# Kernel optimization log

Measured on AMD Instinct MI355X. Metric: run time of the kernel, lower is better.

## Reference

```python
import jax, jax.numpy as jnp
import numpy as np

D, H, S, L = 256, 512, 32, 2  # latent_dim, hidden_dim, stochastic_dim, n_layers
B, T = 256, 256


def setup_inputs() -> dict:
    key = jax.random.key(0)
    ks = jax.random.split(key, 20)

    def w(k, shape, fan_in):
        return jax.random.uniform(k, shape, jnp.float32, -1.0, 1.0) / np.sqrt(fan_in)

    inp = {
        "latent": jax.random.normal(ks[0], (B, T, D), jnp.float32),
        "hidden": jnp.zeros((L, B, H), jnp.float32),
        "eps": jax.random.normal(ks[1], (B, T, S), jnp.float32),
        # GRU layer 0: input = D + S
        "wih0": w(ks[2], (3 * H, D + S), H), "whh0": w(ks[3], (3 * H, H), H),
        "bih0": w(ks[4], (3 * H,), H), "bhh0": w(ks[5], (3 * H,), H),
        # GRU layer 1: input = H
        "wih1": w(ks[6], (3 * H, H), H), "whh1": w(ks[7], (3 * H, H), H),
        "bih1": w(ks[8], (3 * H,), H), "bhh1": w(ks[9], (3 * H,), H),
        # posterior MLP: (H + D) -> H -> 2S
        "wpost1": w(ks[10], (H, H + D), H + D), "bpost1": w(ks[11], (H,), H + D),
        "wpost2": w(ks[12], (2 * S, H), H), "bpost2": w(ks[13], (2 * S,), H),
        # prior MLP: H -> H -> 2S
        "wprior1": w(ks[14], (H, H), H), "bprior1": w(ks[15], (H,), H),
        "wprior2": w(ks[16], (2 * S, H), H), "bprior2": w(ks[17], (2 * S,), H),
    }
    return inp


def _gru_cell(x, h, wih, whh, bih, bhh):
    gi = x @ wih.T + bih   # [B, 3H]
    gh = h @ whh.T + bhh   # [B, 3H]
    ir, iz, inn = jnp.split(gi, 3, axis=-1)
    hr, hz, hn = jnp.split(gh, 3, axis=-1)
    r = jax.nn.sigmoid(ir + hr)
    z = jax.nn.sigmoid(iz + hz)
    n = jnp.tanh(inn + r * hn)
    return (1.0 - z) * n + z * h


def reference(latent, hidden, eps,
              wih0, whh0, bih0, bhh0, wih1, whh1, bih1, bhh1,
              wpost1, bpost1, wpost2, bpost2, wprior1, bprior1, wprior2, bprior2):
    # scan over time; carry = hidden [L, B, H]
    def step(h, xs):
        x_t, e_t = xs  # [B,D], [B,S]
        post_in = jnp.concatenate([h[-1], x_t], axis=-1)           # [B, H+D]
        pp = jax.nn.relu(post_in @ wpost1.T + bpost1) @ wpost2.T + bpost2
        pm, plv = jnp.split(pp, 2, axis=-1)                        # [B,S] each
        stoch = pm + e_t * jnp.exp(0.5 * plv)                      # reparam sample
        rnn_in = jnp.concatenate([x_t, stoch], axis=-1)            # [B, D+S]
        h0 = _gru_cell(rnn_in, h[0], wih0, whh0, bih0, bhh0)
        h1 = _gru_cell(h0, h[1], wih1, whh1, bih1, bhh1)
        h_new = jnp.stack([h0, h1], axis=0)                        # [L,B,H]
        pr = jax.nn.relu(h1 @ wprior1.T + bprior1) @ wprior2.T + bprior2
        prm, prlv = jnp.split(pr, 2, axis=-1)
        return h_new, (stoch, prm, prlv, pm, plv)

    xs = (jnp.swapaxes(latent, 0, 1), jnp.swapaxes(eps, 0, 1))     # [T,B,*]
    h_final, outs = jax.lax.scan(step, hidden, xs)
    stoch, prm, prlv, pm, plv = (jnp.swapaxes(o, 0, 1) for o in outs)  # [B,T,*]
    return stoch, prm, prlv, pm, plv, h_final
```

## Files before the change

kernel.cpp:

```cpp
#include <hip/hip_runtime.h>
#include <math.h>

#define TID ((int)threadIdx.x)

namespace {

constexpr int Bn = 256, Tn = 256, Dn = 256, Hn = 512, Sn = 32;
constexpr int NOS = 32;
constexpr int JH  = 16;
constexpr int BC  = 32;
constexpr int BTS = Bn * Tn * Sn;
constexpr int OFF_ST   = 0;
constexpr int OFF_PRM  = BTS;
constexpr int OFF_PRLV = 2 * BTS;
constexpr int OFF_PM   = 3 * BTS;
constexpr int OFF_PLV  = 4 * BTS;
constexpr int OFF_HF   = 5 * BTS;
constexpr int BARS_PER_TEAM = 1056;

struct P {
  const float *latent, *hidden, *eps;
  const float *wih0, *whh0, *bih0, *bhh0;
  const float *wih1, *whh1, *bih1, *bhh1;
  const float *wpost1, *bpost1, *wpost2, *bpost2;
  const float *wprior1, *bprior1, *wprior2, *bprior2;
  float *out;
  float *h0, *h1, *ph, *qh, *st;
  unsigned *bars;
};

__device__ __forceinline__ void team_bar(unsigned* slot) {
  __syncthreads();
  if (TID == 0) {
    __threadfence();
    __hip_atomic_fetch_add(slot, 1u, __ATOMIC_RELEASE, __HIP_MEMORY_SCOPE_AGENT);
    while (__hip_atomic_load(slot, __ATOMIC_ACQUIRE, __HIP_MEMORY_SCOPE_AGENT) < 32u) {
      __builtin_amdgcn_s_sleep(1);
    }
  }
  __syncthreads();
}

template<int SHIFT>
__device__ __forceinline__ void stageW48(float (*wT)[52], const float* __restrict__ W,
                                         int K, int k0, int os) {
  constexpr int KQ = 1 << SHIFT;
  const int nf4 = 48 * KQ;
  for (int v = TID; v < nf4; v += 512) {
    const int row = v >> SHIFT;
    const int kq  = v & (KQ - 1);
    const int g = row >> 4, j = row & 15;
    const float4 w = *(const float4*)(W + (size_t)(g * Hn + os * JH + j) * K + k0 + (kq << 2));
    const int kk = kq << 2;
    wT[kk + 0][row] = w.x; wT[kk + 1][row] = w.y;
    wT[kk + 2][row] = w.z; wT[kk + 3][row] = w.w;
  }
}

__device__ __forceinline__ void stageW16(float (*wT)[52], int co, const float* __restrict__ W,
                                         int K, int wrow0, int k0) {
  for (int v = TID; v < 256; v += 512) {
    const int j = v >> 4;
    const int kq = v & 15;
    const float4 w = *(const float4*)(W + (size_t)(wrow0 + j) * K + k0 + (kq << 2));
    const int kk = kq << 2;
    wT[kk + 0][co + j] = w.x; wT[kk + 1][co + j] = w.y;
    wT[kk + 2][co + j] = w.z; wT[kk + 3][co + j] = w.w;
  }
}

template<int SHIFT>
__device__ __forceinline__ void stageX(float (*xc)[68], const float* __restrict__ src,
                                       int rstride, int k0, int bg) {
  constexpr int KQ = 1 << SHIFT;
  const int nf4 = 32 * KQ;
  for (int v = TID; v < nf4; v += 512) {
    const int row = v >> SHIFT;
    const int kq = v & (KQ - 1);
    const float4 x = *(const float4*)(src + (size_t)(bg * BC + row) * rstride + k0 + (kq << 2));
    *(float4*)&xc[row][kq << 2] = x;
  }
}

__device__ __forceinline__ void ghAccum(float* acc, const float (*wT)[52], const float (*xc)[68],
                                        int v, int ka, int kb) {
  const int rp = v >> 3, jp = v & 7;
  const int r0 = rp * 2, c0 = jp * 2;
  #pragma unroll 4
  for (int kk = ka; kk < kb; kk += 2) {
    const float2 xa = *(const float2*)&xc[r0][kk];
    const float2 xb = *(const float2*)&xc[r0 + 1][kk];
    #pragma unroll
    for (int g = 0; g < 3; g++) {
      const float2 w0 = *(const float2*)&wT[kk][g * 16 + c0];
      const float2 w1 = *(const float2*)&wT[kk + 1][g * 16 + c0];
      acc[g * 4 + 0] += xa.x * w0.x + xa.y * w1.x;
      acc[g * 4 + 1] += xa.x * w0.y + xa.y * w1.y;
      acc[g * 4 + 2] += xb.x * w0.x + xb.y * w1.x;
      acc[g * 4 + 3] += xb.x * w0.y + xb.y * w1.y;
    }
  }
}

__device__ __forceinline__ void qAccum(float* acc, const float (*wT)[52], int co,
                                       const float (*xc)[68], int v, int ka, int kb) {
  const int rp = v >> 3, jp = v & 7;
  const int r0 = rp * 2, c0 = jp * 2;
  #pragma unroll 4
  for (int kk = ka; kk < kb; kk += 2) {
    const float2 xa = *(const float2*)&xc[r0][kk];
    const float2 xb = *(const float2*)&xc[r0 + 1][kk];
    const float2 w0 = *(const float2*)&wT[kk][co + c0];
    const float2 w1 = *(const float2*)&wT[kk + 1][co + c0];
    acc[0] += xa.x * w0.x + xa.y * w1.x;
    acc[1] += xa.x * w0.y + xa.y * w1.y;
    acc[2] += xb.x * w0.x + xb.y * w1.x;
    acc[3] += xb.x * w0.y + xb.y * w1.y;
  }
}

__device__ __forceinline__ float dotChunk(const float* __restrict__ x, const float* __restrict__ w,
                                          int k0, int n) {
  float d = 0.f;
  #pragma unroll 4
  for (int k = k0; k < k0 + n; k += 4) {
    const float4 a = *(const float4*)(x + k);
    const float4 b = *(const float4*)(w + k);
    d += a.x * b.x + a.y * b.y + a.z * b.z + a.w * b.w;
  }
  return d;
}

__global__ __launch_bounds__(512, 1) void rssm_kernel(P p) {
  __shared__ float wT0[64][52];
  __shared__ float wT1[64][52];
  __shared__ float xcA[32][68];
  __shared__ float xcB[32][68];
  __shared__ float ghA[32][48];
  __shared__ float ghB[32][48];
  __shared__ float part[4][32][48];
  __shared__ float ppq[2][2][32];
  __shared__ float prq[2][2][32];
  __shared__ float ppv[32][2];

  const int bg = blockIdx.x & 7;
  const int os = blockIdx.x >> 3;
  unsigned* bars = p.bars + bg * BARS_PER_TEAM;
  int bar_i = 0;

  const int wv = TID >> 6;
  const int v  = TID & 127;
  const int wp = TID >> 7;

  {
    const int r = TID >> 4, j = TID & 15;
    const int b = bg * BC + r; const int col = os * JH + j;
    p.h0[b * Hn + col] = p.hidden[b * Hn + col];
    p.h1[b * Hn + col] = p.hidden[Bn * Hn + b * Hn + col];
  }
  team_bar(&bars[bar_i++]);

  auto phaseE = [&](int tnext) {
    float acc[4] = {0.f, 0.f, 0.f, 0.f};
    const bool do_ph = (tnext < Tn);
    const int nch = do_ph ? 12 : 8;
    for (int c = 0; c < nch; c++) {
      const int k0 = c << 6;
      if (c < 8) {
        stageW16(wT0, 0, p.wprior1, Hn, os * JH, k0);
        stageX<4>(xcA, p.h1, Hn, k0, bg);
      } else {
        stageX<4>(xcA, p.latent + (size_t)tnext * Dn, Tn * Dn, k0 - Hn, bg);
      }
      if (do_ph) stageW16(wT0, 16, p.wpost1, Hn + Dn, os * JH, k0);
      __syncthreads();
      if (wp < 2) { if (c < 8) qAccum(acc, wT0, 0, xcA, v, wp * 32, wp * 32 + 32); }
      else if (do_ph) qAccum(acc, wT0, 16, xcA, v, (wp - 2) * 32, (wp - 2) * 32 + 32);
      __syncthreads();
    }
    float* pE = &part[0][0][0];
    {
      const int rp = v >> 3, jp = v & 7;
      pE[(wp * 32 + rp * 2    ) * 16 + jp * 2    ] = acc[0];
      pE[(wp * 32 + rp * 2    ) * 16 + jp * 2 + 1] = acc[1];
      pE[(wp * 32 + rp * 2 + 1) * 16 + jp * 2    ] = acc[2];
      pE[(wp * 32 + rp * 2 + 1) * 16 + jp * 2 + 1] = acc[3];
    }
    __syncthreads();
    {
      const int r = TID >> 4, j = TID & 15;
      const int b = bg * BC + r; const int col = os * JH + j;
      const float qv = pE[r * 16 + j] + pE[(32 + r) * 16 + j] + p.bprior1[col];
      p.qh[b * Hn + col] = fmaxf(qv, 0.f);
      if (do_ph) {
        const float pv = pE[(64 + r) * 16 + j] + pE[(96 + r) * 16 + j] + p.bpost1[col];
        p.ph[b * Hn + col] = fmaxf(pv, 0.f);
      }
    }
    __syncthreads();
  };

  auto phaseB = [&](int t) {
    float acc[12] = {0,0,0,0,0,0,0,0,0,0,0,0};
    float dacc = 0.f;
    const int ll = TID & 127;
    const int r_ = ll & 31, cc_ = (ll >> 5) & 1, ks_ = ll >> 6;
    for (int c = 0; c < 8; c++) {
      const int k0 = c << 6;
      stageW48<4>(wT0, p.whh0, Hn, k0, os);
      stageW48<4>(wT1, p.whh1, Hn, k0, os);
      stageX<4>(xcA, p.h0, Hn, k0, bg);
      stageX<4>(xcB, p.h1, Hn, k0, bg);
      __syncthreads();
      if (wv < 2)      ghAccum(acc, wT0, xcA, v, 0, 64);
      else if (wv < 4) ghAccum(acc, wT1, xcB, v, 0, 64);
      else if (wv < 6)
        dacc += dotChunk(p.ph + (size_t)(bg * BC + r_) * Hn,
                         p.wpost2 + (size_t)(os + 32 * cc_) * Hn, ks_ * 256 + c * 32, 32);
      else if (t >= 1)
        dacc += dotChunk(p.qh + (size_t)(bg * BC + r_) * Hn,
                         p.wprior2 + (size_t)(os + 32 * cc_) * Hn, ks_ * 256 + c * 32, 32);
      __syncthreads();
    }
    if (wv < 4) {
      const int rp = v >> 3, jp = v & 7;
      float (*gh)[48] = (wv < 2) ? ghA : ghB;
      const float* bias = (wv < 2) ? p.bhh0 : p.bhh1;
      #pragma unroll
      for (int g = 0; g < 3; g++) {
        const int col = os * JH + jp * 2;
        gh[rp * 2    ][g * 16 + jp * 2    ] = acc[g * 4 + 0] + bias[g * Hn + col];
        gh[rp * 2    ][g * 16 + jp * 2 + 1] = acc[g * 4 + 1] + bias[g * Hn + col + 1];
        gh[rp * 2 + 1][g * 16 + jp * 2    ] = acc[g * 4 + 2] + bias[g * Hn + col];
        gh[rp * 2 + 1][g * 16 + jp * 2 + 1] = acc[g * 4 + 3] + bias[g * Hn + col + 1];
      }
    } else if (wv < 6) {
      ppq[cc_][ks_][r_] = dacc;
    } else if (t >= 1) {
      prq[cc_][ks_][r_] = dacc;
    }
    __syncthreads();
    if (TID < 64) {
      const int r = TID & 31, cc = TID >> 5;
      ppv[r][cc] = ppq[cc][0][r] + ppq[cc][1][r] + p.bpost2[os + 32 * cc];
    } else if (TID < 128 && t >= 1) {
      const int u = TID - 64; const int r = u & 31, cc = u >> 5;
      const float val = prq[cc][0][r] + prq[cc][1][r] + p.bprior2[os + 32 * cc];
      p.out[(cc ? OFF_PRLV : OFF_PRM) + (size_t)(bg * BC + r) * (Tn * Sn) + (t - 1) * Sn + os] = val;
    }
    __syncthreads();
    if (TID < 32) {
      const int r = TID; const int b = bg * BC + r;
      const float pm = ppv[r][0], plv = ppv[r][1];
      const float e = p.eps[(size_t)b * (Tn * Sn) + t * Sn + os];
      const float sv = pm + e * expf(0.5f * plv);
      p.st[b * Sn + os] = sv;
      p.out[OFF_ST  + (size_t)b * (Tn * Sn) + t * Sn + os] = sv;
      p.out[OFF_PM  + (size_t)b * (Tn * Sn) + t * Sn + os] = pm;
      p.out[OFF_PLV + (size_t)b * (Tn * Sn) + t * Sn + os] = plv;
    }
    __syncthreads();
  };

  auto phaseGRU = [&](const float* W, const float* bih, float (*ghL)[48], float* hbuf,
                      bool layer0, int t) {
    float acc[12] = {0,0,0,0,0,0,0,0,0,0,0,0};
    const int nch = layer0 ? 5 : 8;
    for (int c = 0; c < nch; c++) {
      const int k0 = c << 6;
      int klen;
      if (layer0) {
        if (c < 4) { stageW48<4>(wT0, W, Dn + Sn, k0, os);
                     stageX<4>(xcA, p.latent + (size_t)t * Dn, Tn * Dn, k0, bg); klen = 64; }
        else       { stageW48<3>(wT0, W, Dn + Sn, k0, os);
                     stageX<3>(xcA, p.st, Sn, 0, bg); klen = 32; }
      } else {
        stageW48<4>(wT0, W, Hn, k0, os);
        stageX<4>(xcA, p.h0, Hn, k0, bg); klen = 64;
      }
      __syncthreads();
      const int q = klen >> 2;
      ghAccum(acc, wT0, xcA, v, wp * q, wp * q + q);
      __syncthreads();
    }
    {
      const int rp = v >> 3, jp = v & 7;
      #pragma unroll
      for (int g = 0; g < 3; g++) {
        part[wp][rp * 2    ][g * 16 + jp * 2    ] = acc[g * 4 + 0];
        part[wp][rp * 2    ][g * 16 + jp * 2 + 1] = acc[g * 4 + 1];
        part[wp][rp * 2 + 1][g * 16 + jp * 2    ] = acc[g * 4 + 2];
        part[wp][rp * 2 + 1][g * 16 + jp * 2 + 1] = acc[g * 4 + 3];
      }
    }
    __syncthreads();
    {
      const int r = TID >> 4, j = TID & 15;
      const int b = bg * BC + r; const int col = os * JH + j;
      const float ig0 = part[0][r][j] + part[1][r][j] + part[2][r][j] + part[3][r][j] + bih[col];
      const float ig1 = part[0][r][16 + j] + part[1][r][16 + j] + part[2][r][16 + j] + part[3][r][16 + j] + bih[Hn + col];
      const float ig2 = part[0][r][32 + j] + part[1][r][32 + j] + part[2][r][32 + j] + part[3][r][32 + j] + bih[2 * Hn + col];
      const float hr = ghL[r][j], hz = ghL[r][16 + j], hn = ghL[r][32 + j];
      const float rg = 1.f / (1.f + expf(-(ig0 + hr)));
      const float zg = 1.f / (1.f + expf(-(ig1 + hz)));
      const float ng = tanhf(ig2 + rg * hn);
      const float hold = hbuf[b * Hn + col];
      hbuf[b * Hn + col] = (1.f - zg) * ng + zg * hold;
    }
    __syncthreads();
  };

  phaseE(0);
  team_bar(&bars[bar_i++]);

  for (int t = 0; t < Tn; t++) {
    phaseB(t);
    team_bar(&bars[bar_i++]);
    phaseGRU(p.wih0, p.bih0, ghA, p.h0, true, t);
    team_bar(&bars[bar_i++]);
    phaseGRU(p.wih1, p.bih1, ghB, p.h1, false, t);
    team_bar(&bars[bar_i++]);
    phaseE(t + 1);
    team_bar(&bars[bar_i++]);
  }

  {
    const int ll = TID & 127;
    const int r_ = ll & 31, cc_ = (ll >> 5) & 1, ks_ = ll >> 6;
    if (wv >= 6) {
      const float d = dotChunk(p.qh + (size_t)(bg * BC + r_) * Hn,
                               p.wprior2 + (size_t)(os + 32 * cc_) * Hn, ks_ * 256, 256);
      prq[cc_][ks_][r_] = d;
    }
    __syncthreads();
    if (TID >= 64 && TID < 128) {
      const int u = TID - 64; const int r = u & 31, cc = u >> 5;
      const float val = prq[cc][0][r] + prq[cc][1][r] + p.bprior2[os + 32 * cc];
      p.out[(cc ? OFF_PRLV : OFF_PRM) + (size_t)(bg * BC + r) * (Tn * Sn) + 255 * Sn + os] = val;
    }
    const int r = TID >> 4, j = TID & 15;
    const int b = bg * BC + r; const int col = os * JH + j;
    p.out[OFF_HF + b * Hn + col] = p.h0[b * Hn + col];
    p.out[OFF_HF + Bn * Hn + b * Hn + col] = p.h1[b * Hn + col];
  }
}

}

extern "C" void kernel_launch(void* const* d_in, const int* in_sizes, int n_in,
                              void* d_out, int out_size, void* d_ws, size_t ws_size,
                              hipStream_t stream) {
  (void)in_sizes; (void)n_in; (void)out_size; (void)ws_size;
  float* ws = (float*)d_ws;
  P p;
  p.latent  = (const float*)d_in[0];
  p.hidden  = (const float*)d_in[1];
  p.eps     = (const float*)d_in[2];
  p.wih0    = (const float*)d_in[3];
  p.whh0    = (const float*)d_in[4];
  p.bih0    = (const float*)d_in[5];
  p.bhh0    = (const float*)d_in[6];
  p.wih1    = (const float*)d_in[7];
  p.whh1    = (const float*)d_in[8];
  p.bih1    = (const float*)d_in[9];
  p.bhh1    = (const float*)d_in[10];
  p.wpost1  = (const float*)d_in[11];
  p.bpost1  = (const float*)d_in[12];
  p.wpost2  = (const float*)d_in[13];
  p.bpost2  = (const float*)d_in[14];
  p.wprior1 = (const float*)d_in[15];
  p.bprior1 = (const float*)d_in[16];
  p.wprior2 = (const float*)d_in[17];
  p.bprior2 = (const float*)d_in[18];
  p.out = (float*)d_out;
  p.h0 = ws;
  p.h1 = ws + 131072;
  p.ph = ws + 262144;
  p.qh = ws + 393216;
  p.st = ws + 524288;
  p.bars = (unsigned*)(ws + 532480);

  hipMemsetAsync(p.bars, 0, 8 * BARS_PER_TEAM * sizeof(unsigned), stream);

  void* args[] = { &p };
  hipLaunchCooperativeKernel((void*)rssm_kernel, dim3(256), dim3(512), args, 0, stream);
}
```

Baseline: 33.18 ms.

## Keep per-block weight slices resident in LDS and restructure team partitioning

Repartitions the work so each of 256 blocks owns 4 hidden columns for one of 2 batch halves of 128 rows. All of that block's weight slices (GRU input and hidden weights, post/prior first layers, one head row) are preloaded into dynamic LDS once, instead of being restaged from global memory every chunk of every timestep. Activations are streamed in 32-wide chunks that are double-buffered through registers, and the K split is reduced with a shuffle butterfly. The per-step flat atomic barrier with a fresh slot each time is replaced by a two-level tree barrier that counts epochs. The trade-off is a large LDS footprint and a 128-block team spin barrier, which may cost more synchronisation latency.

```diff
diff --git a/kernel.cpp b/kernel.cpp
--- a/kernel.cpp
+++ b/kernel.cpp
@@ -6,17 +6,25 @@
 namespace {
 
 constexpr int Bn = 256, Tn = 256, Dn = 256, Hn = 512, Sn = 32;
-constexpr int NOS = 32;
-constexpr int JH  = 16;
-constexpr int BC  = 32;
+constexpr int BC = 128;
+constexpr int XP = 268;
+constexpr int CHF = 16 * XP;
 constexpr int BTS = Bn * Tn * Sn;
-constexpr int OFF_ST   = 0;
-constexpr int OFF_PRM  = BTS;
-constexpr int OFF_PRLV = 2 * BTS;
-constexpr int OFF_PM   = 3 * BTS;
-constexpr int OFF_PLV  = 4 * BTS;
-constexpr int OFF_HF   = 5 * BTS;
-constexpr int BARS_PER_TEAM = 1056;
+constexpr int OFF_ST = 0, OFF_PRM = BTS, OFF_PRLV = 2 * BTS, OFF_PM = 3 * BTS,
+              OFF_PLV = 4 * BTS, OFF_HF = 5 * BTS;
+
+constexpr int oWH0 = 0;
+constexpr int oWH1 = oWH0 + 512 * 12;
+constexpr int oWI1 = oWH1 + 512 * 12;
+constexpr int oWI0 = oWI1 + 512 * 12;
+constexpr int oWP1 = oWI0 + 288 * 12;
+constexpr int oWQ1 = oWP1 + 768 * 4;
+constexpr int oWHD = oWQ1 + 512 * 4;
+constexpr int oGA  = oWHD + 512;
+constexpr int oGB  = oGA + 128 * 12;
+constexpr int oXT  = oGB + 128 * 12;
+constexpr int LDS_FLOATS = oXT + 2 * CHF;
+constexpr int LDS_BYTES  = LDS_FLOATS * 4;
 
 struct P {
   const float *latent, *hidden, *eps;
@@ -25,323 +33,395 @@
   const float *wpost1, *bpost1, *wpost2, *bpost2;
   const float *wprior1, *bprior1, *wprior2, *bprior2;
   float *out;
-  float *h0, *h1, *ph, *qh, *st;
+  float *h0, *h1, *ph, *qh, *ppv;
   unsigned *bars;
 };
 
-__device__ __forceinline__ void team_bar(unsigned* slot) {
+struct F4x2 { float4 a, b; };
+struct SR { float4 pm0, pm1, lv0, lv1, e0, e1; };
+
+__device__ __forceinline__ void team_bar(const P& p, int bg, int grp, int e) {
   __syncthreads();
   if (TID == 0) {
-    __threadfence();
-    __hip_atomic_fetch_add(slot, 1u, __ATOMIC_RELEASE, __HIP_MEMORY_SCOPE_AGENT);
-    while (__hip_atomic_load(slot, __ATOMIC_ACQUIRE, __HIP_MEMORY_SCOPE_AGENT) < 32u) {
-      __builtin_amdgcn_s_sleep(1);
-    }
+    unsigned* leaf = p.bars + bg * 8 + grp;
+    unsigned* root = p.bars + 16 + bg;
+    unsigned* rel  = p.bars + 18 + bg;
+    unsigned old = __hip_atomic_fetch_add(leaf, 1u, __ATOMIC_RELEASE, __HIP_MEMORY_SCOPE_AGENT);
+    if ((old & 15u) == 15u) {
+      unsigned r = __hip_atomic_fetch_add(root, 1u, __ATOMIC_ACQ_REL, __HIP_MEMORY_SCOPE_AGENT);
+      if ((r & 7u) == 7u)
+        __hip_atomic_store(rel, (unsigned)e, __ATOMIC_RELEASE, __HIP_MEMORY_SCOPE_AGENT);
+    }
+    while (__hip_atomic_load(rel, __ATOMIC_RELAXED, __HIP_MEMORY_SCOPE_AGENT) < (unsigned)e)
+      __builtin_amdgcn_s_sleep(2);
+    (void)__hip_atomic_load(rel, __ATOMIC_ACQUIRE, __HIP_MEMORY_SCOPE_AGENT);
   }
   __syncthreads();
 }
 
-template<int SHIFT>
-__device__ __forceinline__ void stageW48(float (*wT)[52], const float* __restrict__ W,
-                                         int K, int k0, int os) {
-  constexpr int KQ = 1 << SHIFT;
-  const int nf4 = 48 * KQ;
-  for (int v = TID; v < nf4; v += 512) {
-    const int row = v >> SHIFT;
-    const int kq  = v & (KQ - 1);
-    const int g = row >> 4, j = row & 15;
-    const float4 w = *(const float4*)(W + (size_t)(g * Hn + os * JH + j) * K + k0 + (kq << 2));
-    const int kk = kq << 2;
-    wT[kk + 0][row] = w.x; wT[kk + 1][row] = w.y;
-    wT[kk + 2][row] = w.z; wT[kk + 3][row] = w.w;
-  }
-}
-
-__device__ __forceinline__ void stageW16(float (*wT)[52], int co, const float* __restrict__ W,
-                                         int K, int wrow0, int k0) {
-  for (int v = TID; v < 256; v += 512) {
-    const int j = v >> 4;
-    const int kq = v & 15;
-    const float4 w = *(const float4*)(W + (size_t)(wrow0 + j) * K + k0 + (kq << 2));
-    const int kk = kq << 2;
-    wT[kk + 0][co + j] = w.x; wT[kk + 1][co + j] = w.y;
-    wT[kk + 2][co + j] = w.z; wT[kk + 3][co + j] = w.w;
-  }
-}
-
-template<int SHIFT>
-__device__ __forceinline__ void stageX(float (*xc)[68], const float* __restrict__ src,
-                                       int rstride, int k0, int bg) {
-  constexpr int KQ = 1 << SHIFT;
-  const int nf4 = 32 * KQ;
-  for (int v = TID; v < nf4; v += 512) {
-    const int row = v >> SHIFT;
-    const int kq = v & (KQ - 1);
-    const float4 x = *(const float4*)(src + (size_t)(bg * BC + row) * rstride + k0 + (kq << 2));
-    *(float4*)&xc[row][kq << 2] = x;
-  }
-}
-
-__device__ __forceinline__ void ghAccum(float* acc, const float (*wT)[52], const float (*xc)[68],
-                                        int v, int ka, int kb) {
-  const int rp = v >> 3, jp = v & 7;
-  const int r0 = rp * 2, c0 = jp * 2;
-  #pragma unroll 4
-  for (int kk = ka; kk < kb; kk += 2) {
-    const float2 xa = *(const float2*)&xc[r0][kk];
-    const float2 xb = *(const float2*)&xc[r0 + 1][kk];
-    #pragma unroll
-    for (int g = 0; g < 3; g++) {
-      const float2 w0 = *(const float2*)&wT[kk][g * 16 + c0];
-      const float2 w1 = *(const float2*)&wT[kk + 1][g * 16 + c0];
-      acc[g * 4 + 0] += xa.x * w0.x + xa.y * w1.x;
-      acc[g * 4 + 1] += xa.x * w0.y + xa.y * w1.y;
-      acc[g * 4 + 2] += xb.x * w0.x + xb.y * w1.x;
-      acc[g * 4 + 3] += xb.x * w0.y + xb.y * w1.y;
-    }
-  }
-}
-
-__device__ __forceinline__ void qAccum(float* acc, const float (*wT)[52], int co,
-                                       const float (*xc)[68], int v, int ka, int kb) {
-  const int rp = v >> 3, jp = v & 7;
-  const int r0 = rp * 2, c0 = jp * 2;
-  #pragma unroll 4
-  for (int kk = ka; kk < kb; kk += 2) {
-    const float2 xa = *(const float2*)&xc[r0][kk];
-    const float2 xb = *(const float2*)&xc[r0 + 1][kk];
-    const float2 w0 = *(const float2*)&wT[kk][co + c0];
-    const float2 w1 = *(const float2*)&wT[kk + 1][co + c0];
-    acc[0] += xa.x * w0.x + xa.y * w1.x;
-    acc[1] += xa.x * w0.y + xa.y * w1.y;
-    acc[2] += xb.x * w0.x + xb.y * w1.x;
-    acc[3] += xb.x * w0.y + xb.y * w1.y;
-  }
-}
-
-__device__ __forceinline__ float dotChunk(const float* __restrict__ x, const float* __restrict__ w,
-                                          int k0, int n) {
-  float d = 0.f;
-  #pragma unroll 4
-  for (int k = k0; k < k0 + n; k += 4) {
-    const float4 a = *(const float4*)(x + k);
-    const float4 b = *(const float4*)(w + k);
-    d += a.x * b.x + a.y * b.y + a.z * b.z + a.w * b.w;
-  }
-  return d;
-}
-
-__global__ __launch_bounds__(512, 1) void rssm_kernel(P p) {
-  __shared__ float wT0[64][52];
-  __shared__ float wT1[64][52];
-  __shared__ float xcA[32][68];
-  __shared__ float xcB[32][68];
-  __shared__ float ghA[32][48];
-  __shared__ float ghB[32][48];
-  __shared__ float part[4][32][48];
-  __shared__ float ppq[2][2][32];
-  __shared__ float prq[2][2][32];
-  __shared__ float ppv[32][2];
-
-  const int bg = blockIdx.x & 7;
-  const int os = blockIdx.x >> 3;
-  unsigned* bars = p.bars + bg * BARS_PER_TEAM;
-  int bar_i = 0;
-
-  const int wv = TID >> 6;
-  const int v  = TID & 127;
-  const int wp = TID >> 7;
-
+template<int K>
+__device__ void preload12(float* wt, const float* __restrict__ W, int os) {
+  constexpr int KQ = K / 4;
+  for (int u = TID; u < 12 * KQ; u += 512) {
+    int c = u / KQ, kq = u - c * KQ;
+    int row = (c >> 2) * Hn + os * 4 + (c & 3);
+    float4 w = *(const float4*)(W + (size_t)row * K + kq * 4);
+    int k = kq * 4;
+    wt[(k + 0) * 12 + c] = w.x; wt[(k + 1) * 12 + c] = w.y;
+    wt[(k + 2) * 12 + c] = w.z; wt[(k + 3) * 12 + c] = w.w;
+  }
+}
+template<int K>
+__device__ void preload4(float* wt, const float* __restrict__ W, int os) {
+  constexpr int KQ = K / 4;
+  for (int u = TID; u < 4 * KQ; u += 512) {
+    int c = u / KQ, kq = u - c * KQ;
+    int row = os * 4 + c;
+    float4 w = *(const float4*)(W + (size_t)row * K + kq * 4);
+    int k = kq * 4;
+    wt[(k + 0) * 4 + c] = w.x; wt[(k + 1) * 4 + c] = w.y;
+    wt[(k + 2) * 4 + c] = w.z; wt[(k + 3) * 4 + c] = w.w;
+  }
+}
+
+__device__ __forceinline__ F4x2 stLoad(const float* __restrict__ src, size_t ld, int k0) {
+  F4x2 v;
+  const int r0 = TID >> 3, kq = TID & 7;
+  v.a = *(const float4*)(src + (size_t)r0 * ld + k0 + kq * 4);
+  v.b = *(const float4*)(src + (size_t)(r0 + 64) * ld + k0 + kq * 4);
+  return v;
+}
+__device__ __forceinline__ void stWrite(float* __restrict__ xb, const F4x2& v) {
+  const int r0 = TID >> 3, kq = TID & 7;
+  *(float2*)&xb[(2 * kq) * XP + 2 * r0]       = make_float2(v.a.x, v.a.y);
+  *(float2*)&xb[(2 * kq + 1) * XP + 2 * r0]   = make_float2(v.a.z, v.a.w);
+  *(float2*)&xb[(2 * kq) * XP + 2 * (r0 + 64)]     = make_float2(v.b.x, v.b.y);
+  *(float2*)&xb[(2 * kq + 1) * XP + 2 * (r0 + 64)] = make_float2(v.b.z, v.b.w);
+}
+
+__device__ __forceinline__ void mm12(float* __restrict__ acc, const float* __restrict__ xb,
+                                     const float* __restrict__ wt, int rp, int ks) {
+  const float4 xa = *(const float4*)&xb[ks * XP + rp * 8];
+  const float4 xc = *(const float4*)&xb[ks * XP + rp * 8 + 4];
+  const float* w = wt + ks * 24;
+  float wA[12], wB[12];
+  #pragma unroll
+  for (int c = 0; c < 12; c += 4) {
+    *(float4*)&wA[c] = *(const float4*)&w[c];
+    *(float4*)&wB[c] = *(const float4*)&w[12 + c];
+  }
+  const float x0[4] = {xa.x, xa.z, xc.x, xc.z};
+  const float x1[4] = {xa.y, xa.w, xc.y, xc.w};
+  #pragma unroll
+  for (int ri = 0; ri < 4; ri++)
+    #pragma unroll
+    for (int c = 0; c < 12; c++)
+      acc[ri * 12 + c] += x0[ri] * wA[c] + x1[ri] * wB[c];
+}
+
+template<bool DP>
+__device__ __forceinline__ void mmE(float* __restrict__ acc, const float* __restrict__ xb,
+                                    const float* __restrict__ wq, const float* __restrict__ wp,
+                                    int rp, int ks) {
+  const float4 xa = *(const float4*)&xb[ks * XP + rp * 8];
+  const float4 xc = *(const float4*)&xb[ks * XP + rp * 8 + 4];
+  const float x0[4] = {xa.x, xa.z, xc.x, xc.z};
+  const float x1[4] = {xa.y, xa.w, xc.y, xc.w};
+  const float4 q0 = *(const float4*)&wq[ks * 8];
+  const float4 q1 = *(const float4*)&wq[ks * 8 + 4];
+  const float qA[4] = {q0.x, q0.y, q0.z, q0.w};
+  const float qB[4] = {q1.x, q1.y, q1.z, q1.w};
+  float pA[4] = {0, 0, 0, 0}, pB[4] = {0, 0, 0, 0};
+  if (DP) {
+    const float4 p0 = *(const float4*)&wp[ks * 8];
+    const float4 p1 = *(const float4*)&wp[ks * 8 + 4];
+    pA[0] = p0.x; pA[1] = p0.y; pA[2] = p0.z; pA[3] = p0.w;
+    pB[0] = p1.x; pB[1] = p1.y; pB[2] = p1.z; pB[3] = p1.w;
+  }
+  #pragma unroll
+  for (int ri = 0; ri < 4; ri++)
+    #pragma unroll
+    for (int c = 0; c < 4; c++) {
+      acc[ri * 8 + c] += x0[ri] * qA[c] + x1[ri] * qB[c];
+      if (DP) acc[ri * 8 + 4 + c] += x0[ri] * pA[c] + x1[ri] * pB[c];
+    }
+}
+
+__device__ __forceinline__ void mmEpost(float* __restrict__ acc, const float* __restrict__ xb,
+                                        const float* __restrict__ wp, int rp, int ks) {
+  const float4 xa = *(const float4*)&xb[ks * XP + rp * 8];
+  const float4 xc = *(const float4*)&xb[ks * XP + rp * 8 + 4];
+  const float x0[4] = {xa.x, xa.z, xc.x, xc.z};
+  const float x1[4] = {xa.y, xa.w, xc.y, xc.w};
+  const float4 p0 = *(const float4*)&wp[ks * 8];
+  const float4 p1 = *(const float4*)&wp[ks * 8 + 4];
+  const float pA[4] = {p0.x, p0.y, p0.z, p0.w};
+  const float pB[4] = {p1.x, p1.y, p1.z, p1.w};
+  #pragma unroll
+  for (int ri = 0; ri < 4; ri++)
+    #pragma unroll
+    for (int c = 0; c < 4; c++)
+      acc[ri * 8 + 4 + c] += x0[ri] * pA[c] + x1[ri] * pB[c];
+}
+
+template<int N>
+__device__ __forceinline__ void bfly(float* acc) {
+  #pragma unroll
+  for (int m = 1; m <= 8; m <<= 1)
+    #pragma unroll
+    for (int i = 0; i < N; i++)
+      acc[i] += __shfl_xor(acc[i], m, 64);
+}
+
+__global__ __launch_bounds__(512, 2) void rssm_kernel(P p) {
+  extern __shared__ float sm[];
+  const int bg = blockIdx.x & 1;
+  const int os = blockIdx.x >> 1;
+  const int grp = os & 7;
+  const int rp = TID >> 4, ks = TID & 15;
+  int ep = 0;
+
+  float* WH0 = sm + oWH0; float* WH1 = sm + oWH1; float* WI1 = sm + oWI1;
+  float* WI0 = sm + oWI0; float* WP1 = sm + oWP1; float* WQ1 = sm + oWQ1;
+  float* WHD = sm + oWHD; float* GA = sm + oGA;  float* GB = sm + oGB;
+  auto XT = [&](int i) { return sm + oXT + i * CHF; };
+
+  preload12<512>(WH0, p.whh0, os);
+  preload12<512>(WH1, p.whh1, os);
+  preload12<512>(WI1, p.wih1, os);
+  preload12<288>(WI0, p.wih0, os);
+  preload4<768>(WP1, p.wpost1, os);
+  preload4<512>(WQ1, p.wprior1, os);
   {
-    const int r = TID >> 4, j = TID & 15;
-    const int b = bg * BC + r; const int col = os * JH + j;
-    p.h0[b * Hn + col] = p.hidden[b * Hn + col];
-    p.h1[b * Hn + col] = p.hidden[Bn * Hn + b * Hn + col];
-  }
-  team_bar(&bars[bar_i++]);
-
-  auto phaseE = [&](int tnext) {
-    float acc[4] = {0.f, 0.f, 0.f, 0.f};
-    const bool do_ph = (tnext < Tn);
-    const int nch = do_ph ? 12 : 8;
+    const float* hw = (os < 64) ? (p.wpost2 + (size_t)os * Hn)
+                                : (p.wprior2 + (size_t)(os - 64) * Hn);
+    for (int u = TID; u < 128; u += 512)
+      *(float4*)&WHD[u * 4] = *(const float4*)(hw + u * 4);
+  }
+  {
+    const int r = TID >> 2, j = TID & 3;
+    const int b = bg * BC + r, col = os * 4 + j;
+    p.h0[(size_t)b * Hn + col] = p.hidden[(size_t)b * Hn + col];
+    p.h1[(size_t)b * Hn + col] = p.hidden[(size_t)Bn * Hn + b * Hn + col];
+  }
+  team_bar(p, bg, grp, ++ep);
+
+  auto runMM12 = [&](float* acc, const float* src, size_t ld, const float* wt, int nch) {
+    F4x2 nxt;
+    { F4x2 cur = stLoad(src, ld, 0);
+      if (nch > 1) nxt = stLoad(src, ld, 32);
+      stWrite(XT(0), cur); }
+    __syncthreads();
     for (int c = 0; c < nch; c++) {
-      const int k0 = c << 6;
-      if (c < 8) {
-        stageW16(wT0, 0, p.wprior1, Hn, os * JH, k0);
-        stageX<4>(xcA, p.h1, Hn, k0, bg);
+      F4x2 fut;
+      if (c + 2 < nch) fut = stLoad(src, ld, (c + 2) * 32);
+      mm12(acc, XT(c & 1), wt + c * 32 * 12, rp, ks);
+      if (c + 1 < nch) stWrite(XT((c + 1) & 1), nxt);
+      __syncthreads();
+      nxt = fut;
+    }
+  };
+
+  auto writeG = [&](float* G, const float* acc, const float* bhh) {
+    if (ks < 12) {
+      const int c = ks, g = c >> 2, j = c & 3;
+      const float bb = bhh[g * Hn + os * 4 + j];
+      #pragma unroll
+      for (int i = 0; i < 4; i++) G[(rp * 4 + i) * 12 + c] = acc[i * 12 + c] + bb;
+    }
+  };
+
+  auto combine = [&](const float* acc, const float* G, float* hbuf, const float* bih) {
+    if (ks < 4) {
+      const int j = ks, col = os * 4 + j;
+      const float b0 = bih[col], b1 = bih[Hn + col], b2 = bih[2 * Hn + col];
+      #pragma unroll
+      for (int i = 0; i < 4; i++) {
+        const int r = rp * 4 + i, b = bg * BC + r;
+        const float gr = acc[i * 12 + j] + b0 + G[r * 12 + j];
+        const float gz = acc[i * 12 + 4 + j] + b1 + G[r * 12 + 4 + j];
+        const float gn = acc[i * 12 + 8 + j] + b2;
+        const float hnv = G[r * 12 + 8 + j];
+        const float rg = 1.f / (1.f + expf(-gr));
+        const float zg = 1.f / (1.f + expf(-gz));
+        const float ng = tanhf(gn + rg * hnv);
+        const size_t idx = (size_t)b * Hn + col;
+        hbuf[idx] = (1.f - zg) * ng + zg * hbuf[idx];
+      }
+    }
+  };
+
+  auto headPhase = [&](int t, bool post) {
+    const int r = TID >> 2, kq = TID & 3;
+    const int b = bg * BC + r;
+    const float* xs = (post ? p.ph : p.qh) + (size_t)b * Hn;
+    float d = 0.f;
+    #pragma unroll
+    for (int q = 0; q < 32; q++) {
+      const int k = kq * 128 + q * 4;
+      const float4 xv = *(const float4*)(xs + k);
+      const float4 wv = *(const float4*)&WHD[k];
+      d += xv.x * wv.x + xv.y * wv.y + xv.z * wv.z + xv.w * wv.w;
+    }
+    d += __shfl_xor(d, 1, 64);
+    d += __shfl_xor(d, 2, 64);
+    if (kq == 0) {
+      if (post) {
+        const float val = d + p.bpost2[os];
+        p.ppv[(size_t)b * 64 + os] = val;
+        const size_t o = ((size_t)b * Tn + t) * Sn + (os & 31);
+        p.out[(os < 32 ? OFF_PM : OFF_PLV) + o] = val;
       } else {
-        stageX<4>(xcA, p.latent + (size_t)tnext * Dn, Tn * Dn, k0 - Hn, bg);
+        const int cc = os - 64;
+        const float val = d + p.bprior2[cc];
+        const size_t o = ((size_t)b * Tn + (t - 1)) * Sn + (cc & 31);
+        p.out[(cc < 32 ? OFF_PRM : OFF_PRLV) + o] = val;
       }
-      if (do_ph) stageW16(wT0, 16, p.wpost1, Hn + Dn, os * JH, k0);
+    }
+  };
+
+  auto stochLoad = [&](SR& s, int t) {
+    const int r = TID >> 2, sq = TID & 3;
+    const int b = bg * BC + r;
+    const float* pv = p.ppv + (size_t)b * 64;
+    s.pm0 = *(const float4*)(pv + sq * 8);
+    s.pm1 = *(const float4*)(pv + sq * 8 + 4);
+    s.lv0 = *(const float4*)(pv + 32 + sq * 8);
+    s.lv1 = *(const float4*)(pv + 32 + sq * 8 + 4);
+    const float* epp = p.eps + ((size_t)b * Tn + t) * Sn + sq * 8;
+    s.e0 = *(const float4*)epp;
+    s.e1 = *(const float4*)(epp + 4);
+  };
+  auto stochWrite = [&](float* xb, const SR& s, int t) {
+    const int r = TID >> 2, sq = TID & 3;
+    const int b = bg * BC + r;
+    const float pm[8] = {s.pm0.x, s.pm0.y, s.pm0.z, s.pm0.w, s.pm1.x, s.pm1.y, s.pm1.z, s.pm1.w};
+    const float lv[8] = {s.lv0.x, s.lv0.y, s.lv0.z, s.lv0.w, s.lv1.x, s.lv1.y, s.lv1.z, s.lv1.w};
+    const float ev[8] = {s.e0.x, s.e0.y, s.e0.z, s.e0.w, s.e1.x, s.e1.y, s.e1.z, s.e1.w};
+    float sv[8];
+    #pragma unroll
+    for (int u = 0; u < 8; u++) sv[u] = pm[u] + ev[u] * expf(0.5f * lv[u]);
+    #pragma unroll
+    for (int up = 0; up < 4; up++) {
+      const int s2 = sq * 4 + up;
+      *(float2*)&xb[s2 * XP + 2 * r] = make_float2(sv[up * 2], sv[up * 2 + 1]);
+    }
+    if (os == 0) {
+      #pragma unroll
+      for (int u = 0; u < 8; u++)
+        p.out[OFF_ST + ((size_t)b * Tn + t) * Sn + sq * 8 + u] = sv[u];
+    }
+  };
+
+  auto phaseE = [&](int tn) {
+    const bool dp = (tn < Tn);
+    const int nch = dp ? 24 : 16;
+    const float* s1 = p.h1 + (size_t)bg * BC * Hn;
+    const float* slat = p.latent + (size_t)bg * BC * (size_t)(Tn * Dn) + (size_t)(dp ? tn : 0) * Dn;
+    auto eload = [&](int c) -> F4x2 {
+      return (c < 16) ? stLoad(s1, Hn, c * 32)
+                      : stLoad(slat, (size_t)Tn * Dn, (c - 16) * 32);
+    };
+    float acc[32] = {};
+    F4x2 nxt;
+    { F4x2 cur = eload(0); nxt = eload(1); stWrite(XT(0), cur); }
+    __syncthreads();
+    for (int c = 0; c < nch; c++) {
+      F4x2 fut;
+      if (c + 2 < nch) fut = eload(c + 2);
+      const float* xb = XT(c & 1);
+      if (c < 16) {
+        if (dp) mmE<true>(acc, xb, WQ1 + c * 32 * 4, WP1 + c * 32 * 4, rp, ks);
+        else    mmE<false>(acc, xb, WQ1 + c * 32 * 4, nullptr, rp, ks);
+      } else {
+        mmEpost(acc, xb, WP1 + c * 32 * 4, rp, ks);
+      }
+      if (c + 1 < nch) stWrite(XT((c + 1) & 1), nxt);
       __syncthreads();
-      if (wp < 2) { if (c < 8) qAccum(acc, wT0, 0, xcA, v, wp * 32, wp * 32 + 32); }
-      else if (do_ph) qAccum(acc, wT0, 16, xcA, v, (wp - 2) * 32, (wp - 2) * 32 + 32);
+      nxt = fut;
+    }
+    bfly<32>(acc);
+    if (ks < 4) {
+      const int col = os * 4 + ks;
+      const float bq = p.bprior1[col];
+      #pragma unroll
+      for (int i = 0; i < 4; i++)
+        p.qh[(size_t)(bg * BC + rp * 4 + i) * Hn + col] = fmaxf(acc[i * 8 + ks] + bq, 0.f);
+    } else if (ks < 8 && dp) {
+      const int j = ks - 4, col = os * 4 + j;
+      const float bp = p.bpost1[col];
+      #pragma unroll
+      for (int i = 0; i < 4; i++)
+        p.ph[(size_t)(bg * BC + rp * 4 + i) * Hn + col] = fmaxf(acc[i * 8 + 4 + j] + bp, 0.f);
+    }
+  };
+
+  auto phaseB = [&](int t) {
+    {
+      float acc[48] = {};
+      runMM12(acc, p.h0 + (size_t)bg * BC * Hn, Hn, WH0, 16);
+      bfly<48>(acc);
+      writeG(GA, acc, p.bhh0);
+    }
+    {
+      float acc[48] = {};
+      runMM12(acc, p.h1 + (size_t)bg * BC * Hn, Hn, WH1, 16);
+      bfly<48>(acc);
+      writeG(GB, acc, p.bhh1);
+    }
+    if (os < 64) headPhase(t, true);
+    else if (t >= 1) headPhase(t, false);
+  };
+
+  auto phaseC = [&](int t) {
+    const float* slat = p.latent + (size_t)bg * BC * (size_t)(Tn * Dn) + (size_t)t * Dn;
+    const size_t ldl = (size_t)Tn * Dn;
+    float acc[48] = {};
+    SR sreg;
+    F4x2 nxt;
+    { F4x2 cur = stLoad(slat, ldl, 0); nxt = stLoad(slat, ldl, 32); stWrite(XT(0), cur); }
+    __syncthreads();
+    for (int c = 0; c <= 8; c++) {
+      F4x2 fut;
+      if (c + 2 < 8) fut = stLoad(slat, ldl, (c + 2) * 32);
+      else if (c + 2 == 8) stochLoad(sreg, t);
+      mm12(acc, XT(c & 1), WI0 + c * 32 * 12, rp, ks);
+      if (c + 1 < 8) stWrite(XT((c + 1) & 1), nxt);
+      else if (c + 1 == 8) stochWrite(XT(0), sreg, t);
       __syncthreads();
-    }
-    float* pE = &part[0][0][0];
-    {
-      const int rp = v >> 3, jp = v & 7;
-      pE[(wp * 32 + rp * 2    ) * 16 + jp * 2    ] = acc[0];
-      pE[(wp * 32 + rp * 2    ) * 16 + jp * 2 + 1] = acc[1];
-      pE[(wp * 32 + rp * 2 + 1) * 16 + jp * 2    ] = acc[2];
-      pE[(wp * 32 + rp * 2 + 1) * 16 + jp * 2 + 1] = acc[3];
-    }
-    __syncthreads();
-    {
-      const int r = TID >> 4, j = TID & 15;
-      const int b = bg * BC + r; const int col = os * JH + j;
-      const float qv = pE[r * 16 + j] + pE[(32 + r) * 16 + j] + p.bprior1[col];
-      p.qh[b * Hn + col] = fmaxf(qv, 0.f);
-      if (do_ph) {
-        const float pv = pE[(64 + r) * 16 + j] + pE[(96 + r) * 16 + j] + p.bpost1[col];
-        p.ph[b * Hn + col] = fmaxf(pv, 0.f);
-      }
-    }
-    __syncthreads();
-  };
-
-  auto phaseB = [&](int t) {
-    float acc[12] = {0,0,0,0,0,0,0,0,0,0,0,0};
-    float dacc = 0.f;
-    const int ll = TID & 127;
-    const int r_ = ll & 31, cc_ = (ll >> 5) & 1, ks_ = ll >> 6;
-    for (int c = 0; c < 8; c++) {
-      const int k0 = c << 6;
-      stageW48<4>(wT0, p.whh0, Hn, k0, os);
-      stageW48<4>(wT1, p.whh1, Hn, k0, os);
-      stageX<4>(xcA, p.h0, Hn, k0, bg);
-      stageX<4>(xcB, p.h1, Hn, k0, bg);
-      __syncthreads();
-      if (wv < 2)      ghAccum(acc, wT0, xcA, v, 0, 64);
-      else if (wv < 4) ghAccum(acc, wT1, xcB, v, 0, 64);
-      else if (wv < 6)
-        dacc += dotChunk(p.ph + (size_t)(bg * BC + r_) * Hn,
-                         p.wpost2 + (size_t)(os + 32 * cc_) * Hn, ks_ * 256 + c * 32, 32);
-      else if (t >= 1)
-        dacc += dotChunk(p.qh + (size_t)(bg * BC + r_) * Hn,
-                         p.wprior2 + (size_t)(os + 32 * cc_) * Hn, ks_ * 256 + c * 32, 32);
-      __syncthreads();
-    }
-    if (wv < 4) {
-      const int rp = v >> 3, jp = v & 7;
-      float (*gh)[48] = (wv < 2) ? ghA : ghB;
-      const float* bias = (wv < 2) ? p.bhh0 : p.bhh1;
-      #pragma unroll
-      for (int g = 0; g < 3; g++) {
-        const int col = os * JH + jp * 2;
-        gh[rp * 2    ][g * 16 + jp * 2    ] = acc[g * 4 + 0] + bias[g * Hn + col];
-        gh[rp * 2    ][g * 16 + jp * 2 + 1] = acc[g * 4 + 1] + bias[g * Hn + col + 1];
-        gh[rp * 2 + 1][g * 16 + jp * 2    ] = acc[g * 4 + 2] + bias[g * Hn + col];
-        gh[rp * 2 + 1][g * 16 + jp * 2 + 1] = acc[g * 4 + 3] + bias[g * Hn + col + 1];
-      }
-    } else if (wv < 6) {
-      ppq[cc_][ks_][r_] = dacc;
-    } else if (t >= 1) {
-      prq[cc_][ks_][r_] = dacc;
-    }
-    __syncthreads();
-    if (TID < 64) {
-      const int r = TID & 31, cc = TID >> 5;
-      ppv[r][cc] = ppq[cc][0][r] + ppq[cc][1][r] + p.bpost2[os + 32 * cc];
-    } else if (TID < 128 && t >= 1) {
-      const int u = TID - 64; const int r = u & 31, cc = u >> 5;
-      const float val = prq[cc][0][r] + prq[cc][1][r] + p.bprior2[os + 32 * cc];
-      p.out[(cc ? OFF_PRLV : OFF_PRM) + (size_t)(bg * BC + r) * (Tn * Sn) + (t - 1) * Sn + os] = val;
-    }
-    __syncthreads();
-    if (TID < 32) {
-      const int r = TID; const int b = bg * BC + r;
-      const float pm = ppv[r][0], plv = ppv[r][1];
-      const float e = p.eps[(size_t)b * (Tn * Sn) + t * Sn + os];
-      const float sv = pm + e * expf(0.5f * plv);
-      p.st[b * Sn + os] = sv;
-      p.out[OFF_ST  + (size_t)b * (Tn * Sn) + t * Sn + os] = sv;
-      p.out[OFF_PM  + (size_t)b * (Tn * Sn) + t * Sn + os] = pm;
-      p.out[OFF_PLV + (size_t)b * (Tn * Sn) + t * Sn + os] = plv;
-    }
-    __syncthreads();
-  };
-
-  auto phaseGRU = [&](const float* W, const float* bih, float (*ghL)[48], float* hbuf,
-                      bool layer0, int t) {
-    float acc[12] = {0,0,0,0,0,0,0,0,0,0,0,0};
-    const int nch = layer0 ? 5 : 8;
-    for (int c = 0; c < nch; c++) {
-      const int k0 = c << 6;
-      int klen;
-      if (layer0) {
-        if (c < 4) { stageW48<4>(wT0, W, Dn + Sn, k0, os);
-                     stageX<4>(xcA, p.latent + (size_t)t * Dn, Tn * Dn, k0, bg); klen = 64; }
-        else       { stageW48<3>(wT0, W, Dn + Sn, k0, os);
-                     stageX<3>(xcA, p.st, Sn, 0, bg); klen = 32; }
-      } else {
-        stageW48<4>(wT0, W, Hn, k0, os);
-        stageX<4>(xcA, p.h0, Hn, k0, bg); klen = 64;
-      }
-      __syncthreads();
-      const int q = klen >> 2;
-      ghAccum(acc, wT0, xcA, v, wp * q, wp * q + q);
-      __syncthreads();
-    }
-    {
-      const int rp = v >> 3, jp = v & 7;
-      #pragma unroll
-      for (int g = 0; g < 3; g++) {
-        part[wp][rp * 2    ][g * 16 + jp * 2    ] = acc[g * 4 + 0];
-        part[wp][rp * 2    ][g * 16 + jp * 2 + 1] = acc[g * 4 + 1];
-        part[wp][rp * 2 + 1][g * 16 + jp * 2    ] = acc[g * 4 + 2];
-        part[wp][rp * 2 + 1][g * 16 + jp * 2 + 1] = acc[g * 4 + 3];
-      }
-    }
-    __syncthreads();
-    {
-      const int r = TID >> 4, j = TID & 15;
-      const int b = bg * BC + r; const int col = os * JH + j;
-      const float ig0 = part[0][r][j] + part[1][r][j] + part[2][r][j] + part[3][r][j] + bih[col];
-      const float ig1 = part[0][r][16 + j] + part[1][r][16 + j] + part[2][r][16 + j] + part[3][r][16 + j] + bih[Hn + col];
-      const float ig2 = part[0][r][32 + j] + part[1][r][32 + j] + part[2][r][32 + j] + part[3][r][32 + j] + bih[2 * Hn + col];
-      const float hr = ghL[r][j], hz = ghL[r][16 + j], hn = ghL[r][32 + j];
-      const float rg = 1.f / (1.f + expf(-(ig0 + hr)));
-      const float zg = 1.f / (1.f + expf(-(ig1 + hz)));
-      const float ng = tanhf(ig2 + rg * hn);
-      const float hold = hbuf[b * Hn + col];
-      hbuf[b * Hn + col] = (1.f - zg) * ng + zg * hold;
-    }
-    __syncthreads();
+      nxt = fut;
+    }
+    bfly<48>(acc);
+    combine(acc, GA, p.h0, p.bih0);
+  };
+
+  auto phaseD = [&]() {
+    float acc[48] = {};
+    runMM12(acc, p.h0 + (size_t)bg * BC * Hn, Hn, WI1, 16);
+    bfly<48>(acc);
+    combine(acc, GB, p.h1, p.bih1);
   };
 
   phaseE(0);
-  team_bar(&bars[bar_i++]);
+  team_bar(p, bg, grp, ++ep);
 
   for (int t = 0; t < Tn; t++) {
     phaseB(t);
-    team_bar(&bars[bar_i++]);
-    phaseGRU(p.wih0, p.bih0, ghA, p.h0, true, t);
-    team_bar(&bars[bar_i++]);
-    phaseGRU(p.wih1, p.bih1, ghB, p.h1, false, t);
-    team_bar(&bars[bar_i++]);
+    team_bar(p, bg, grp, ++ep);
+    phaseC(t);
+    team_bar(p, bg, grp, ++ep);
+    phaseD();
+    team_bar(p, bg, grp, ++ep);
     phaseE(t + 1);
-    team_bar(&bars[bar_i++]);
-  }
-
+    team_bar(p, bg, grp, ++ep);
+  }
+
+  if (os >= 64) headPhase(256, false);
   {
-    const int ll = TID & 127;
-    const int r_ = ll & 31, cc_ = (ll >> 5) & 1, ks_ = ll >> 6;
-    if (wv >= 6) {
-      const float d = dotChunk(p.qh + (size_t)(bg * BC + r_) * Hn,
-                               p.wprior2 + (size_t)(os + 32 * cc_) * Hn, ks_ * 256, 256);
-      prq[cc_][ks_][r_] = d;
-    }
-    __syncthreads();
-    if (TID >= 64 && TID < 128) {
-      const int u = TID - 64; const int r = u & 31, cc = u >> 5;
-      const float val = prq[cc][0][r] + prq[cc][1][r] + p.bprior2[os + 32 * cc];
-      p.out[(cc ? OFF_PRLV : OFF_PRM) + (size_t)(bg * BC + r) * (Tn * Sn) + 255 * Sn + os] = val;
-    }
-    const int r = TID >> 4, j = TID & 15;
-    const int b = bg * BC + r; const int col = os * JH + j;
-    p.out[OFF_HF + b * Hn + col] = p.h0[b * Hn + col];
-    p.out[OFF_HF + Bn * Hn + b * Hn + col] = p.h1[b * Hn + col];
+    const int r = TID >> 2, j = TID & 3;
+    const int b = bg * BC + r, col = os * 4 + j;
+    p.out[OFF_HF + (size_t)b * Hn + col] = p.h0[(size_t)b * Hn + col];
+    p.out[OFF_HF + (size_t)Bn * Hn + (size_t)b * Hn + col] = p.h1[(size_t)b * Hn + col];
   }
 }
 
@@ -373,15 +453,21 @@
   p.wprior2 = (const float*)d_in[17];
   p.bprior2 = (const float*)d_in[18];
   p.out = (float*)d_out;
-  p.h0 = ws;
-  p.h1 = ws + 131072;
-  p.ph = ws + 262144;
-  p.qh = ws + 393216;
-  p.st = ws + 524288;
-  p.bars = (unsigned*)(ws + 532480);
-
-  hipMemsetAsync(p.bars, 0, 8 * BARS_PER_TEAM * sizeof(unsigned), stream);
+  p.h0  = ws;
+  p.h1  = ws + 131072;
+  p.ph  = ws + 262144;
+  p.qh  = ws + 393216;
+  p.ppv = ws + 524288;
+  p.bars = (unsigned*)(ws + 540672);
+
+  static bool attr_done_ignored = false;
+  (void)attr_done_ignored;
+  (void)hipFuncSetAttribute((const void*)rssm_kernel,
+                            hipFuncAttributeMaxDynamicSharedMemorySize, LDS_BYTES);
+
+  hipMemsetAsync(p.bars, 0, 128, stream);
 
   void* args[] = { &p };
-  hipLaunchCooperativeKernel((void*)rssm_kernel, dim3(256), dim3(512), args, 0, stream);
-}
+  hipLaunchCooperativeKernel((void*)rssm_kernel, dim3(256), dim3(512), args,
+                             LDS_BYTES, stream);
+}
```

Measured after the change: 120.6 ms. 264% more time.
